# Performance work log

Hardware: AMD Instinct MI355X
Metric: run time of the kernel (lower is better)

Reference implementation:

```python
import jax, jax.numpy as jnp
import numpy as np

N, NFEAT, NHID, NHEADS, NCLASS = 8192, 512, 64, 8, 40
ALPHA = 0.2
NEG = jnp.float32(-9e15)


def _gat_layer(h, W, a, concat):
    # h: [N, Fin], W: [Fin, Fout], a: [2*Fout, 1]
    Fout = W.shape[1]
    Wh = h @ W                      # [N, Fout]
    f1 = Wh @ a[:Fout]              # [N, 1]
    f2 = Wh @ a[Fout:]              # [N, 1]
    e = jax.nn.leaky_relu(f1 + f2.T, negative_slope=ALPHA)  # [N, N]
    # NOTE: source masks on e > 0 (adj is NOT used) - replicate faithfully
    att = jax.nn.softmax(jnp.where(e > 0, e, NEG), axis=1)
    h_prime = att @ Wh              # [N, Fout]
    return jax.nn.elu(h_prime) if concat else h_prime


def setup_inputs() -> dict:
    key = jax.random.key(0)
    ks = jax.random.split(key, 6)
    x = jax.random.normal(ks[0], (N, NFEAT), dtype=jnp.float32)
    adj = jax.random.randint(ks[1], (N, N), 0, 2).astype(jnp.bool_)  # unused by math, kept for fidelity
    s = 0.1
    W_heads = jax.random.normal(ks[2], (NHEADS, NFEAT, NHID), dtype=jnp.float32) * s
    a_heads = jax.random.normal(ks[3], (NHEADS, 2 * NHID, 1), dtype=jnp.float32) * s
    W_out = jax.random.normal(ks[4], (NHID * NHEADS, NCLASS), dtype=jnp.float32) * s
    a_out = jax.random.normal(ks[5], (2 * NCLASS, 1), dtype=jnp.float32) * s
    return {"x": x, "adj": adj, "W_heads": W_heads, "a_heads": a_heads,
            "W_out": W_out, "a_out": a_out}


def reference(x, adj, W_heads, a_heads, W_out, a_out):
    # multi-head GAT layers (concat=True), vmapped over heads
    heads = jax.vmap(lambda W, a: _gat_layer(x, W, a, True))(W_heads, a_heads)  # [H, N, NHID]
    h = jnp.transpose(heads, (1, 0, 2)).reshape(N, NHEADS * NHID)
    # output attention layer (concat=False), then elu + log_softmax
    out = _gat_layer(h, W_out, a_out, False)
    out = jax.nn.elu(out)
    return jax.nn.log_softmax(out, axis=1)
```

## Files before the change

### kernel.cpp

```cpp
#include <hip/hip_runtime.h>
#include <math.h>

#define N_NODES 8192
#define NFEAT 512
#define NHID 64
#define NHEADS 8
#define NCLASS 40
#define NCHUNK 128
#define CHUNK 64
#define NB 4096

using bf16x8 = __attribute__((ext_vector_type(8))) short;
using f32x4 = __attribute__((ext_vector_type(4))) float;

__device__ __forceinline__ ushort f2b(float f) {
  uint u = __builtin_bit_cast(uint, f);
  u += 0x7FFFu + ((u >> 16) & 1u);
  return (ushort)(u >> 16);
}
__device__ __forceinline__ float b2f(ushort h) {
  uint u = (uint)h << 16;
  return __builtin_bit_cast(float, u);
}
__device__ __forceinline__ uint encf(float f) {
  uint u = __builtin_bit_cast(uint, f);
  return u ^ ((u >> 31) ? 0xFFFFFFFFu : 0x80000000u);
}
__device__ __forceinline__ float decf(uint u) {
  u ^= ((u >> 31) ? 0x80000000u : 0xFFFFFFFFu);
  return __builtin_bit_cast(float, u);
}
__device__ __forceinline__ float3 load_rng(const uint* mm, int head) {
  float h = decf(mm[head * 2]);
  float l = decf(~mm[head * 2 + 1]);
  float scale = (float)NB / fmaxf(h - l, 1e-30f);
  return make_float3(l, scale, h);
}
__device__ __forceinline__ int bucket_of(float v, float lo, float scale) {
  float u = fminf(fmaxf((v - lo) * scale, 0.f), (float)(NB - 1));
  return (int)u;
}

__global__ __launch_bounds__(256) void prep_k(const float* __restrict__ W_heads,
                                              ushort* __restrict__ bth,
                                              ushort* __restrict__ btl,
                                              float* __restrict__ zbase,
                                              int zcount) {
  int gid = blockIdx.x * 256 + threadIdx.x;
  int n = gid >> 9, c = gid & 511;
  int h = n >> 6, f = n & 63;
  float w = W_heads[((size_t)h * NFEAT + c) * NHID + f];
  ushort hh = f2b(w);
  bth[gid] = hh;
  btl[gid] = f2b(w - b2f(hh));
  if (gid < zcount) zbase[gid] = 0.f;
}

__global__ __launch_bounds__(256) void gemm1_k(const float* __restrict__ x,
                                               const ushort* __restrict__ bth,
                                               const ushort* __restrict__ btl,
                                               const float* __restrict__ a_heads,
                                               float* __restrict__ Wh,
                                               float* __restrict__ f1,
                                               float* __restrict__ f2,
                                               float* __restrict__ meanS,
                                               uint* __restrict__ mm1) {
  const int row0 = blockIdx.x * 128, col0 = blockIdx.y * 128;
  const int tid = threadIdx.x;
  const int wave = tid >> 6, lane = tid & 63;
  const int wr = wave >> 1, wc = wave & 1;
  __shared__ ushort Ah[128 * 40], Al[128 * 40], Bh[128 * 40], Bl[128 * 40];
  __shared__ float cs[2][64];
  __shared__ uint lmax[2], lmin[2];
  if (tid < 2) { lmax[tid] = 0u; lmin[tid] = 0u; }
  if (tid < 128) cs[tid >> 6][tid & 63] = 0.f;
  f32x4 acc[4][4] = {};
  const int sr = tid >> 1, sh = (tid & 1) * 16;
  const int fr = lane & 15, quad = lane >> 4;
  for (int k0 = 0; k0 < NFEAT; k0 += 32) {
    {
      const float* xs = x + (size_t)(row0 + sr) * NFEAT + k0 + sh;
      float av[16];
      *reinterpret_cast<float4*>(&av[0])  = *reinterpret_cast<const float4*>(xs);
      *reinterpret_cast<float4*>(&av[4])  = *reinterpret_cast<const float4*>(xs + 4);
      *reinterpret_cast<float4*>(&av[8])  = *reinterpret_cast<const float4*>(xs + 8);
      *reinterpret_cast<float4*>(&av[12]) = *reinterpret_cast<const float4*>(xs + 12);
      uint uh[8], ul[8];
#pragma unroll
      for (int q = 0; q < 8; ++q) {
        ushort h0 = f2b(av[2 * q]), h1 = f2b(av[2 * q + 1]);
        ushort l0 = f2b(av[2 * q] - b2f(h0)), l1 = f2b(av[2 * q + 1] - b2f(h1));
        uh[q] = (uint)h0 | ((uint)h1 << 16);
        ul[q] = (uint)l0 | ((uint)l1 << 16);
      }
      *reinterpret_cast<uint4*>(&Ah[sr * 40 + sh])     = make_uint4(uh[0], uh[1], uh[2], uh[3]);
      *reinterpret_cast<uint4*>(&Ah[sr * 40 + sh + 8]) = make_uint4(uh[4], uh[5], uh[6], uh[7]);
      *reinterpret_cast<uint4*>(&Al[sr * 40 + sh])     = make_uint4(ul[0], ul[1], ul[2], ul[3]);
      *reinterpret_cast<uint4*>(&Al[sr * 40 + sh + 8]) = make_uint4(ul[4], ul[5], ul[6], ul[7]);
      size_t boff = (size_t)(col0 + sr) * NFEAT + k0 + sh;
      *reinterpret_cast<uint4*>(&Bh[sr * 40 + sh])     = *reinterpret_cast<const uint4*>(bth + boff);
      *reinterpret_cast<uint4*>(&Bh[sr * 40 + sh + 8]) = *reinterpret_cast<const uint4*>(bth + boff + 8);
      *reinterpret_cast<uint4*>(&Bl[sr * 40 + sh])     = *reinterpret_cast<const uint4*>(btl + boff);
      *reinterpret_cast<uint4*>(&Bl[sr * 40 + sh + 8]) = *reinterpret_cast<const uint4*>(btl + boff + 8);
    }
    __syncthreads();
    bf16x8 afh[4], afl[4], bfh[4], bfl[4];
#pragma unroll
    for (int q = 0; q < 4; ++q) {
      afh[q] = *reinterpret_cast<const bf16x8*>(&Ah[(wr * 64 + q * 16 + fr) * 40 + quad * 8]);
      afl[q] = *reinterpret_cast<const bf16x8*>(&Al[(wr * 64 + q * 16 + fr) * 40 + quad * 8]);
      bfh[q] = *reinterpret_cast<const bf16x8*>(&Bh[(wc * 64 + q * 16 + fr) * 40 + quad * 8]);
      bfl[q] = *reinterpret_cast<const bf16x8*>(&Bl[(wc * 64 + q * 16 + fr) * 40 + quad * 8]);
    }
#pragma unroll
    for (int qr = 0; qr < 4; ++qr)
#pragma unroll
      for (int qc = 0; qc < 4; ++qc) {
        acc[qr][qc] = __builtin_amdgcn_mfma_f32_16x16x32_bf16(afl[qr], bfh[qc], acc[qr][qc], 0, 0, 0);
        acc[qr][qc] = __builtin_amdgcn_mfma_f32_16x16x32_bf16(afh[qr], bfl[qc], acc[qr][qc], 0, 0, 0);
        acc[qr][qc] = __builtin_amdgcn_mfma_f32_16x16x32_bf16(afh[qr], bfh[qc], acc[qr][qc], 0, 0, 0);
      }
    __syncthreads();
  }
  const int head = blockIdx.y * 2 + wc;
#pragma unroll
  for (int qr = 0; qr < 4; ++qr)
#pragma unroll
    for (int qc = 0; qc < 4; ++qc)
#pragma unroll
      for (int i = 0; i < 4; ++i) {
        int row = row0 + wr * 64 + qr * 16 + quad * 4 + i;
        int col = col0 + wc * 64 + qc * 16 + fr;
        Wh[(size_t)row * NFEAT + col] = acc[qr][qc][i];
      }
  const float* ah = a_heads + head * 2 * NHID;
  float a1v[4], a2v[4];
#pragma unroll
  for (int qc = 0; qc < 4; ++qc) { a1v[qc] = ah[qc * 16 + fr]; a2v[qc] = ah[NHID + qc * 16 + fr]; }
#pragma unroll
  for (int qr = 0; qr < 4; ++qr)
#pragma unroll
    for (int i = 0; i < 4; ++i) {
      float s1 = 0.f, s2 = 0.f;
#pragma unroll
      for (int qc = 0; qc < 4; ++qc) { s1 += acc[qr][qc][i] * a1v[qc]; s2 += acc[qr][qc][i] * a2v[qc]; }
#pragma unroll
      for (int m = 1; m < 16; m <<= 1) { s1 += __shfl_xor(s1, m, 64); s2 += __shfl_xor(s2, m, 64); }
      if (fr == 0) {
        int row = row0 + wr * 64 + qr * 16 + quad * 4 + i;
        f1[(head << 13) + row] = s1;
        f2[(head << 13) + row] = s2;
        atomicMax(&lmax[wc], encf(s2));
        atomicMax(&lmin[wc], ~encf(s2));
      }
    }
#pragma unroll
  for (int qc = 0; qc < 4; ++qc) {
    float v = 0.f;
#pragma unroll
    for (int qr = 0; qr < 4; ++qr)
#pragma unroll
      for (int i = 0; i < 4; ++i) v += acc[qr][qc][i];
    v += __shfl_xor(v, 16, 64);
    v += __shfl_xor(v, 32, 64);
    if (quad == 0) atomicAdd(&cs[wc][qc * 16 + fr], v);
  }
  __syncthreads();
  if (tid < 128) atomicAdd(&meanS[(blockIdx.y * 2 + (tid >> 6)) * NHID + (tid & 63)], cs[tid >> 6][tid & 63]);
  if (tid < 2) {
    atomicMax(&mm1[(blockIdx.y * 2 + tid) * 2], lmax[tid]);
    atomicMax(&mm1[(blockIdx.y * 2 + tid) * 2 + 1], lmin[tid]);
  }
}

__global__ __launch_bounds__(256) void gemm2_k(const float* __restrict__ H,
                                               const float* __restrict__ Wout,
                                               const float* __restrict__ a_out,
                                               float* __restrict__ Wh2,
                                               float* __restrict__ f1b,
                                               float* __restrict__ f2b,
                                               float* __restrict__ meanS2,
                                               uint* __restrict__ mm2) {
  const int row0 = blockIdx.x * 32;
  const int tid = threadIdx.x;
  __shared__ float As[32][33];
  __shared__ float Bs[32][40];
  __shared__ float cs[NCLASS];
  __shared__ uint lmax, lmin;
  if (tid < NCLASS) cs[tid] = 0.f;
  if (tid == 0) { lmax = 0u; lmin = 0u; }
  const int m = tid >> 3;
  const int n0 = (tid & 7) * 5;
  float acc[5] = {};
  for (int k0 = 0; k0 < NFEAT; k0 += 32) {
    {
      int kk = tid & 31, mq = tid >> 5;
#pragma unroll
      for (int r = 0; r < 4; ++r)
        As[kk][mq * 4 + r] = H[(size_t)(row0 + mq * 4 + r) * NFEAT + k0 + kk];
    }
    {
#pragma unroll
      for (int r = 0; r < 5; ++r) {
        int idx = tid + r * 256;
        if (idx < 1280) {
          int c = idx / 40, n = idx - c * 40;
          Bs[c][n] = Wout[(size_t)(k0 + c) * NCLASS + n];
        }
      }
    }
    __syncthreads();
#pragma unroll
    for (int kk = 0; kk < 32; ++kk) {
      float a = As[kk][m];
#pragma unroll
      for (int q = 0; q < 5; ++q) acc[q] += a * Bs[kk][n0 + q];
    }
    __syncthreads();
  }
#pragma unroll
  for (int q = 0; q < 5; ++q) Wh2[(size_t)(row0 + m) * NCLASS + n0 + q] = acc[q];
  float p1 = 0.f, p2 = 0.f;
#pragma unroll
  for (int q = 0; q < 5; ++q) {
    p1 += acc[q] * a_out[n0 + q];
    p2 += acc[q] * a_out[NCLASS + n0 + q];
  }
  p1 += __shfl_xor(p1, 1, 64); p1 += __shfl_xor(p1, 2, 64); p1 += __shfl_xor(p1, 4, 64);
  p2 += __shfl_xor(p2, 1, 64); p2 += __shfl_xor(p2, 2, 64); p2 += __shfl_xor(p2, 4, 64);
  if ((tid & 7) == 0) {
    f1b[row0 + m] = p1;
    f2b[row0 + m] = p2;
    atomicMax(&lmax, encf(p2));
    atomicMax(&lmin, ~encf(p2));
  }
#pragma unroll
  for (int q = 0; q < 5; ++q) atomicAdd(&cs[n0 + q], acc[q]);
  __syncthreads();
  if (tid < NCLASS) atomicAdd(&meanS2[tid], cs[tid]);
  if (tid == 0) { atomicMax(&mm2[0], lmax); atomicMax(&mm2[1], lmin); }
}

__global__ __launch_bounds__(256) void hist_k(const float* __restrict__ f2, const uint* __restrict__ mm,
                                              int* __restrict__ hist) {
  int gid = blockIdx.x * 256 + threadIdx.x;
  int head = gid >> 13;
  float3 rg = load_rng(mm, head);
  atomicAdd(&hist[head * NB + bucket_of(f2[gid], rg.x, rg.y)], 1);
}

__global__ __launch_bounds__(1024) void prefix_k(const int* __restrict__ hist, int* __restrict__ bs) {
  __shared__ int sb[NB];
  int head = blockIdx.x, tid = threadIdx.x;
#pragma unroll
  for (int r = 0; r < NB / 1024; ++r) sb[tid + r * 1024] = hist[head * NB + tid + r * 1024];
  __syncthreads();
  for (int st = 1; st < NB; st <<= 1) {
    int v[NB / 1024];
#pragma unroll
    for (int r = 0; r < NB / 1024; ++r) { int i = tid + r * 1024; v[r] = (i >= st) ? sb[i - st] : 0; }
    __syncthreads();
#pragma unroll
    for (int r = 0; r < NB / 1024; ++r) sb[tid + r * 1024] += v[r];
    __syncthreads();
  }
#pragma unroll
  for (int r = 0; r < NB / 1024; ++r) {
    int b = tid + r * 1024;
    bs[head * (NB + 1) + b] = b ? sb[b - 1] : 0;
  }
  if (tid == 0) bs[head * (NB + 1) + NB] = sb[NB - 1];
}

__global__ __launch_bounds__(256) void scat_k(const float* __restrict__ f2, const uint* __restrict__ mm,
                                              const int* __restrict__ bs, int* __restrict__ cnt,
                                              int* __restrict__ idxs, float* __restrict__ f2s,
                                              float* __restrict__ g) {
  int gid = blockIdx.x * 256 + threadIdx.x;
  int head = gid >> 13, i = gid & 8191;
  float v = f2[gid];
  float3 rg = load_rng(mm, head);
  int b = bucket_of(v, rg.x, rg.y);
  int pos = bs[head * (NB + 1) + b] + atomicAdd(&cnt[head * NB + b], 1);
  int base = head << 13;
  idxs[base + pos] = i;
  f2s[base + pos] = v;
  g[base + pos] = expf(v - rg.z);
}

template <int F, int LD, int COLSTEP>
__global__ __launch_bounds__(256) void scanA_k(const float* __restrict__ Wh,
                                               const float* __restrict__ g,
                                               const int* __restrict__ idxs,
                                               float* __restrict__ S,
                                               float* __restrict__ D,
                                               float* __restrict__ T_,
                                               float* __restrict__ Td) {
  constexpr int PAD = (F == 64) ? 66 : 42;
  const int head = blockIdx.y, chunk = blockIdx.x;
  const int tid = threadIdx.x, w = tid >> 6, lane = tid & 63;
  const int base = head << 13;
  const int kbase = base + chunk * CHUNK;
  __shared__ float Sloc[64][PAD];
  __shared__ float Dloc[64];
  __shared__ float wtot[4][PAD];
  __shared__ float wtotD[4];
  int myj = 0; float myg = 0.f;
  if (lane < 16) {
    myj = idxs[kbase + w * 16 + lane];
    myg = g[kbase + w * 16 + lane];
  }
  float acc = 0.f, accD = 0.f;
#pragma unroll
  for (int kk = 15; kk >= 0; --kk) {
    int j = __shfl(myj, kk, 64);
    float gk = __shfl(myg, kk, 64);
    float wv = (lane < F) ? Wh[(size_t)j * LD + head * COLSTEP + lane] : 0.f;
    acc += gk * wv;
    accD += gk;
    if (lane < F) Sloc[w * 16 + kk][lane] = acc;
    if (lane == 0) Dloc[w * 16 + kk] = accD;
  }
  if (lane < F) wtot[w][lane] = acc;
  if (lane == 0) wtotD[w] = accD;
  __syncthreads();
  float off = 0.f, offD = 0.f;
#pragma unroll
  for (int w2 = 1; w2 < 4; ++w2) {
    if (w + w2 < 4) {
      off += (lane < F) ? wtot[w + w2][lane] : 0.f;
      offD += wtotD[w + w2];
    }
  }
#pragma unroll
  for (int kk = 0; kk < 16; ++kk) {
    int e = w * 16 + kk;
    if (lane < F) S[(size_t)(kbase + e) * F + lane] = Sloc[e][lane] + off;
    if (lane == 0) D[kbase + e] = Dloc[e] + offD;
  }
  if (w == 0) {
    if (lane < F) T_[(size_t)(head * NCHUNK + chunk) * F + lane] = wtot[0][lane] + off;
    if (lane == 0) Td[head * NCHUNK + chunk] = wtotD[0] + offD;
  }
}

template <int F>
__global__ __launch_bounds__(1024) void scanB_k(float* __restrict__ T_, float* __restrict__ Td) {
  __shared__ float s[NCHUNK * F];
  __shared__ float td[NCHUNK];
  int head = blockIdx.x;
  int tid = threadIdx.x, slot = tid >> 6, lane = tid & 63;
#pragma unroll
  for (int r = 0; r < 8; ++r) {
    int c = r * 16 + slot;
    if (lane < F) s[c * F + lane] = T_[(size_t)(head * NCHUNK + c) * F + lane];
  }
  if (tid < NCHUNK) td[tid] = Td[head * NCHUNK + tid];
  __syncthreads();
  for (int st = 1; st < NCHUNK; st <<= 1) {
    float v[8];
    float tv = 0.f;
#pragma unroll
    for (int r = 0; r < 8; ++r) {
      int c = r * 16 + slot;
      v[r] = (lane < F && c + st < NCHUNK) ? s[(c + st) * F + lane] : 0.f;
    }
    if (tid < NCHUNK && tid + st < NCHUNK) tv = td[tid + st];
    __syncthreads();
#pragma unroll
    for (int r = 0; r < 8; ++r) {
      int c = r * 16 + slot;
      if (lane < F) s[c * F + lane] += v[r];
    }
    if (tid < NCHUNK) td[tid] += tv;
    __syncthreads();
  }
#pragma unroll
  for (int r = 0; r < 8; ++r) {
    int c = r * 16 + slot;
    if (lane < F) T_[(size_t)(head * NCHUNK + c) * F + lane] = s[c * F + lane];
  }
  if (tid < NCHUNK) Td[head * NCHUNK + tid] = td[tid];
}

__global__ __launch_bounds__(256) void query1_k(const float* __restrict__ f1,
                                                const float* __restrict__ f2s,
                                                const int* __restrict__ idxs,
                                                const float* __restrict__ Wh,
                                                const float* __restrict__ S,
                                                const float* __restrict__ D,
                                                const float* __restrict__ T_,
                                                const float* __restrict__ Td,
                                                const uint* __restrict__ mm,
                                                const int* __restrict__ bs,
                                                const float* __restrict__ meanS,
                                                float* __restrict__ H) {
  int w = blockIdx.x * 4 + (threadIdx.x >> 6);
  int lane = threadIdx.x & 63;
  int head = w & 7, i = w >> 3, base = head << 13;
  float t = f1[base + i];
  float3 rg = load_rng(mm, head);
  int B0 = bucket_of(-t, rg.x, rg.y);
  int p0 = bs[head * (NB + 1) + B0], p1 = bs[head * (NB + 1) + B0 + 1];
  float num = 0.f, den = 0.f;
  int cnt = N_NODES - p1;
  if (p1 < N_NODES) {
    int c = p1 >> 6;
    num = S[(size_t)(base + p1) * NHID + lane] +
          ((c + 1 < NCHUNK) ? T_[(size_t)(head * NCHUNK + c + 1) * NHID + lane] : 0.f);
    den = D[base + p1] + ((c + 1 < NCHUNK) ? Td[head * NCHUNK + c + 1] : 0.f);
  }
  for (int p = p0; p < p1; ++p) {
    float v = f2s[base + p];
    if (t + v > 0.f) {
      int j = idxs[base + p];
      float gk = expf(v - rg.z);
      num += gk * Wh[(size_t)j * NFEAT + head * NHID + lane];
      den += gk;
      ++cnt;
    }
  }
  float val = cnt ? num / den : meanS[head * NHID + lane] * (1.f / N_NODES);
  H[(size_t)i * NFEAT + head * NHID + lane] = (val > 0.f) ? val : expm1f(val);
}

__global__ __launch_bounds__(256) void final_k(const float* __restrict__ f1b,
                                               const float* __restrict__ f2bs,
                                               const int* __restrict__ idx2,
                                               const float* __restrict__ Wh2,
                                               const float* __restrict__ S2,
                                               const float* __restrict__ D2,
                                               const float* __restrict__ T2,
                                               const float* __restrict__ Td2,
                                               const uint* __restrict__ mm2,
                                               const int* __restrict__ bs2,
                                               const float* __restrict__ meanS2,
                                               float* __restrict__ out) {
  int i = blockIdx.x * 4 + (threadIdx.x >> 6);
  int lane = threadIdx.x & 63;
  float t = f1b[i];
  float3 rg = load_rng(mm2, 0);
  int B0 = bucket_of(-t, rg.x, rg.y);
  int p0 = bs2[B0], p1 = bs2[B0 + 1];
  float num = 0.f, den = 0.f;
  int cnt = N_NODES - p1;
  if (p1 < N_NODES) {
    int c = p1 >> 6;
    num = (lane < NCLASS) ? (S2[(size_t)p1 * NCLASS + lane] +
                             ((c + 1 < NCHUNK) ? T2[(size_t)(c + 1) * NCLASS + lane] : 0.f))
                          : 0.f;
    den = D2[p1] + ((c + 1 < NCHUNK) ? Td2[c + 1] : 0.f);
  }
  for (int p = p0; p < p1; ++p) {
    float v = f2bs[p];
    if (t + v > 0.f) {
      int j = idx2[p];
      float gk = expf(v - rg.z);
      if (lane < NCLASS) num += gk * Wh2[(size_t)j * NCLASS + lane];
      den += gk;
      ++cnt;
    }
  }
  float o;
  if (lane < NCLASS) {
    float val = cnt ? num / den : meanS2[lane] * (1.f / N_NODES);
    o = (val > 0.f) ? val : expm1f(val);
  } else {
    o = -INFINITY;
  }
  float m = o;
#pragma unroll
  for (int msk = 32; msk; msk >>= 1) m = fmaxf(m, __shfl_xor(m, msk, 64));
  float e = (lane < NCLASS) ? expf(o - m) : 0.f;
#pragma unroll
  for (int msk = 32; msk; msk >>= 1) e += __shfl_xor(e, msk, 64);
  if (lane < NCLASS) out[(size_t)i * NCLASS + lane] = o - m - logf(e);
}

extern "C" void kernel_launch(void* const* d_in, const int* in_sizes, int n_in,
                              void* d_out, int out_size, void* d_ws, size_t ws_size,
                              hipStream_t stream) {
  const float* x       = (const float*)d_in[0];
  const float* W_heads = (const float*)d_in[2];
  const float* a_heads = (const float*)d_in[3];
  const float* W_out   = (const float*)d_in[4];
  const float* a_out   = (const float*)d_in[5];
  float* out = (float*)d_out;

  float* ws = (float*)d_ws;
  size_t o = 0;
  auto alloc = [&](size_t n) { float* p = ws + o; o += (n + 3) & ~(size_t)3; return p; };
  float*  S1     = alloc((size_t)NHEADS * N_NODES * NHID);
  ushort* BTh    = (ushort*)alloc((size_t)NFEAT * NFEAT / 2);
  ushort* BTl    = (ushort*)alloc((size_t)NFEAT * NFEAT / 2);
  float*  Wh     = alloc((size_t)N_NODES * NFEAT);
  float*  H      = alloc((size_t)N_NODES * NFEAT);
  float*  f1     = alloc(NHEADS * N_NODES);
  float*  f2     = alloc(NHEADS * N_NODES);
  float*  f2s    = alloc(NHEADS * N_NODES);
  int*    idxs   = (int*)alloc(NHEADS * N_NODES);
  float*  g1     = alloc(NHEADS * N_NODES);
  float*  D1     = alloc(NHEADS * N_NODES);
  float*  T1     = alloc(NHEADS * NCHUNK * NHID);
  float*  Td1    = alloc(NHEADS * NCHUNK);
  int*    bst1   = (int*)alloc(NHEADS * (NB + 1));
  float*  Wh2    = alloc((size_t)N_NODES * NCLASS);
  float*  S2     = alloc((size_t)N_NODES * NCLASS);
  float*  f1b    = alloc(N_NODES);
  float*  f2b    = alloc(N_NODES);
  float*  f2bs   = alloc(N_NODES);
  int*    idx2   = (int*)alloc(N_NODES);
  float*  g2     = alloc(N_NODES);
  float*  D2     = alloc(N_NODES);
  float*  T2     = alloc(NCHUNK * NCLASS);
  float*  Td2    = alloc(NCHUNK);
  int*    bst2   = (int*)alloc(NB + 1);
  float*  zbase  = ws + o;
  int*    hist1  = (int*)alloc((size_t)NHEADS * NB);
  int*    cnt1   = (int*)alloc((size_t)NHEADS * NB);
  int*    hist2  = (int*)alloc(NB);
  int*    cnt2   = (int*)alloc(NB);
  uint*   mm1    = (uint*)alloc(16);
  uint*   mm2    = (uint*)alloc(4);
  float*  meanS1 = alloc(NHEADS * NHID);
  float*  meanS2 = alloc(64);
  int zcount = (int)((ws + o) - zbase);

  prep_k<<<1024, 256, 0, stream>>>(W_heads, BTh, BTl, zbase, zcount);
  gemm1_k<<<dim3(64, 4), 256, 0, stream>>>(x, BTh, BTl, a_heads, Wh, f1, f2, meanS1, mm1);
  hist_k<<<(NHEADS * N_NODES) / 256, 256, 0, stream>>>(f2, mm1, hist1);
  prefix_k<<<NHEADS, 1024, 0, stream>>>(hist1, bst1);
  scat_k<<<(NHEADS * N_NODES) / 256, 256, 0, stream>>>(f2, mm1, bst1, cnt1, idxs, f2s, g1);
  scanA_k<NHID, NFEAT, NHID><<<dim3(NCHUNK, NHEADS), 256, 0, stream>>>(Wh, g1, idxs, S1, D1, T1, Td1);
  scanB_k<NHID><<<NHEADS, 1024, 0, stream>>>(T1, Td1);
  query1_k<<<16384, 256, 0, stream>>>(f1, f2s, idxs, Wh, S1, D1, T1, Td1, mm1, bst1, meanS1, H);

  gemm2_k<<<256, 256, 0, stream>>>(H, W_out, a_out, Wh2, f1b, f2b, meanS2, mm2);
  hist_k<<<N_NODES / 256, 256, 0, stream>>>(f2b, mm2, hist2);
  prefix_k<<<1, 1024, 0, stream>>>(hist2, bst2);
  scat_k<<<N_NODES / 256, 256, 0, stream>>>(f2b, mm2, bst2, cnt2, idx2, f2bs, g2);
  scanA_k<NCLASS, NCLASS, 0><<<dim3(NCHUNK, 1), 256, 0, stream>>>(Wh2, g2, idx2, S2, D2, T2, Td2);
  scanB_k<NCLASS><<<1, 1024, 0, stream>>>(T2, Td2);
  final_k<<<2048, 256, 0, stream>>>(f1b, f2bs, idx2, Wh2, S2, D2, T2, Td2, mm2, bst2, meanS2, out);
}
```

Baseline: 535.8 us.

## Fuse histogram/prefix/scatter into one bucket kernel and fold chunk scan via last-block

Replaces the three-kernel bucket sort (global histogram, prefix, scatter) with a single per-head 1024-thread kernel that builds the histogram in shared memory, scans it, and scatters with shared-memory atomics. It also merges the second-level chunk-total scan into the first-level scan kernel, using a threadfence and atomic counter so the last-finishing block does the cross-chunk scan. This removes several launches and global atomic traffic. In exchange, bucketing now runs on only one block per head, which limits parallelism, and the last-block scan is serialized onto a single 256-thread block.

```diff
diff --git a/kernel.cpp b/kernel.cpp
--- a/kernel.cpp
+++ b/kernel.cpp
@@ -241,70 +241,81 @@
   if (tid == 0) { atomicMax(&mm2[0], lmax); atomicMax(&mm2[1], lmin); }
 }
 
-__global__ __launch_bounds__(256) void hist_k(const float* __restrict__ f2, const uint* __restrict__ mm,
-                                              int* __restrict__ hist) {
-  int gid = blockIdx.x * 256 + threadIdx.x;
-  int head = gid >> 13;
+__global__ __launch_bounds__(1024) void bucket_k(const float* __restrict__ f2,
+                                                 const uint* __restrict__ mm,
+                                                 int* __restrict__ bs,
+                                                 int* __restrict__ idxs,
+                                                 float* __restrict__ f2s,
+                                                 float* __restrict__ g) {
+  __shared__ int sb[NB];
+  const int head = blockIdx.x, tid = threadIdx.x;
+  const int base = head * N_NODES;
   float3 rg = load_rng(mm, head);
-  atomicAdd(&hist[head * NB + bucket_of(f2[gid], rg.x, rg.y)], 1);
-}
-
-__global__ __launch_bounds__(1024) void prefix_k(const int* __restrict__ hist, int* __restrict__ bs) {
-  __shared__ int sb[NB];
-  int head = blockIdx.x, tid = threadIdx.x;
-#pragma unroll
-  for (int r = 0; r < NB / 1024; ++r) sb[tid + r * 1024] = hist[head * NB + tid + r * 1024];
+#pragma unroll
+  for (int r = 0; r < NB / 1024; ++r) sb[tid + r * 1024] = 0;
+  __syncthreads();
+  float v[8];
+  int bk[8];
+#pragma unroll
+  for (int r = 0; r < 8; ++r) {
+    v[r] = f2[base + tid + r * 1024];
+    bk[r] = bucket_of(v[r], rg.x, rg.y);
+    atomicAdd(&sb[bk[r]], 1);
+  }
   __syncthreads();
   for (int st = 1; st < NB; st <<= 1) {
-    int v[NB / 1024];
-#pragma unroll
-    for (int r = 0; r < NB / 1024; ++r) { int i = tid + r * 1024; v[r] = (i >= st) ? sb[i - st] : 0; }
-    __syncthreads();
-#pragma unroll
-    for (int r = 0; r < NB / 1024; ++r) sb[tid + r * 1024] += v[r];
-    __syncthreads();
-  }
+    int t[NB / 1024];
+#pragma unroll
+    for (int r = 0; r < NB / 1024; ++r) { int i = tid + r * 1024; t[r] = (i >= st) ? sb[i - st] : 0; }
+    __syncthreads();
+#pragma unroll
+    for (int r = 0; r < NB / 1024; ++r) sb[tid + r * 1024] += t[r];
+    __syncthreads();
+  }
+  int ex[NB / 1024];
 #pragma unroll
   for (int r = 0; r < NB / 1024; ++r) {
     int b = tid + r * 1024;
-    bs[head * (NB + 1) + b] = b ? sb[b - 1] : 0;
+    ex[r] = b ? sb[b - 1] : 0;
+    bs[head * (NB + 1) + b] = ex[r];
   }
   if (tid == 0) bs[head * (NB + 1) + NB] = sb[NB - 1];
-}
-
-__global__ __launch_bounds__(256) void scat_k(const float* __restrict__ f2, const uint* __restrict__ mm,
-                                              const int* __restrict__ bs, int* __restrict__ cnt,
-                                              int* __restrict__ idxs, float* __restrict__ f2s,
-                                              float* __restrict__ g) {
-  int gid = blockIdx.x * 256 + threadIdx.x;
-  int head = gid >> 13, i = gid & 8191;
-  float v = f2[gid];
-  float3 rg = load_rng(mm, head);
-  int b = bucket_of(v, rg.x, rg.y);
-  int pos = bs[head * (NB + 1) + b] + atomicAdd(&cnt[head * NB + b], 1);
-  int base = head << 13;
-  idxs[base + pos] = i;
-  f2s[base + pos] = v;
-  g[base + pos] = expf(v - rg.z);
+  __syncthreads();
+#pragma unroll
+  for (int r = 0; r < NB / 1024; ++r) sb[tid + r * 1024] = ex[r];
+  __syncthreads();
+#pragma unroll
+  for (int r = 0; r < 8; ++r) {
+    int pos = atomicAdd(&sb[bk[r]], 1);
+    int i = tid + r * 1024;
+    idxs[base + pos] = i;
+    f2s[base + pos] = v[r];
+    g[base + pos] = expf(v[r] - rg.z);
+  }
 }
 
 template <int F, int LD, int COLSTEP>
-__global__ __launch_bounds__(256) void scanA_k(const float* __restrict__ Wh,
-                                               const float* __restrict__ g,
-                                               const int* __restrict__ idxs,
-                                               float* __restrict__ S,
-                                               float* __restrict__ D,
-                                               float* __restrict__ T_,
-                                               float* __restrict__ Td) {
+__global__ __launch_bounds__(256) void scanAB_k(const float* __restrict__ Wh,
+                                                const float* __restrict__ g,
+                                                const int* __restrict__ idxs,
+                                                float* __restrict__ S,
+                                                float* __restrict__ D,
+                                                float* __restrict__ T_,
+                                                float* __restrict__ Td,
+                                                int* __restrict__ cntA) {
   constexpr int PAD = (F == 64) ? 66 : 42;
+  constexpr int SZ1 = 64 * PAD + 4 * PAD + 64 + 4;
+  constexpr int SZ2 = NCHUNK * F + NCHUNK;
+  __shared__ float smem[SZ1 > SZ2 ? SZ1 : SZ2];
+  __shared__ int isLast;
+  float (*Sloc)[PAD] = (float(*)[PAD])smem;
+  float* wtot  = smem + 64 * PAD;
+  float* Dloc  = wtot + 4 * PAD;
+  float* wtotD = Dloc + 64;
   const int head = blockIdx.y, chunk = blockIdx.x;
   const int tid = threadIdx.x, w = tid >> 6, lane = tid & 63;
   const int base = head << 13;
   const int kbase = base + chunk * CHUNK;
-  __shared__ float Sloc[64][PAD];
-  __shared__ float Dloc[64];
-  __shared__ float wtot[4][PAD];
-  __shared__ float wtotD[4];
   int myj = 0; float myg = 0.f;
   if (lane < 16) {
     myj = idxs[kbase + w * 16 + lane];
@@ -321,14 +332,14 @@
     if (lane < F) Sloc[w * 16 + kk][lane] = acc;
     if (lane == 0) Dloc[w * 16 + kk] = accD;
   }
-  if (lane < F) wtot[w][lane] = acc;
+  if (lane < F) wtot[w * PAD + lane] = acc;
   if (lane == 0) wtotD[w] = accD;
   __syncthreads();
   float off = 0.f, offD = 0.f;
 #pragma unroll
   for (int w2 = 1; w2 < 4; ++w2) {
     if (w + w2 < 4) {
-      off += (lane < F) ? wtot[w + w2][lane] : 0.f;
+      off += (lane < F) ? wtot[(w + w2) * PAD + lane] : 0.f;
       offD += wtotD[w + w2];
     }
   }
@@ -339,48 +350,37 @@
     if (lane == 0) D[kbase + e] = Dloc[e] + offD;
   }
   if (w == 0) {
-    if (lane < F) T_[(size_t)(head * NCHUNK + chunk) * F + lane] = wtot[0][lane] + off;
+    if (lane < F) T_[(size_t)(head * NCHUNK + chunk) * F + lane] = wtot[lane] + off;
     if (lane == 0) Td[head * NCHUNK + chunk] = wtotD[0] + offD;
   }
-}
-
-template <int F>
-__global__ __launch_bounds__(1024) void scanB_k(float* __restrict__ T_, float* __restrict__ Td) {
-  __shared__ float s[NCHUNK * F];
-  __shared__ float td[NCHUNK];
-  int head = blockIdx.x;
-  int tid = threadIdx.x, slot = tid >> 6, lane = tid & 63;
-#pragma unroll
-  for (int r = 0; r < 8; ++r) {
-    int c = r * 16 + slot;
-    if (lane < F) s[c * F + lane] = T_[(size_t)(head * NCHUNK + c) * F + lane];
-  }
-  if (tid < NCHUNK) td[tid] = Td[head * NCHUNK + tid];
-  __syncthreads();
+  __threadfence();
+  if (tid == 0) isLast = (atomicAdd(&cntA[head], 1) == NCHUNK - 1);
+  __syncthreads();
+  if (!isLast) return;
+  float* s  = smem;
+  float* td = smem + NCHUNK * F;
+  for (int idx = tid; idx < NCHUNK * F; idx += 256) s[idx] = T_[(size_t)head * NCHUNK * F + idx];
+  for (int c = tid; c < NCHUNK; c += 256) td[c] = Td[head * NCHUNK + c];
+  __syncthreads();
+  constexpr int PT = (NCHUNK * F + 255) / 256;
   for (int st = 1; st < NCHUNK; st <<= 1) {
-    float v[8];
-    float tv = 0.f;
-#pragma unroll
-    for (int r = 0; r < 8; ++r) {
-      int c = r * 16 + slot;
-      v[r] = (lane < F && c + st < NCHUNK) ? s[(c + st) * F + lane] : 0.f;
-    }
-    if (tid < NCHUNK && tid + st < NCHUNK) tv = td[tid + st];
-    __syncthreads();
-#pragma unroll
-    for (int r = 0; r < 8; ++r) {
-      int c = r * 16 + slot;
-      if (lane < F) s[c * F + lane] += v[r];
-    }
-    if (tid < NCHUNK) td[tid] += tv;
-    __syncthreads();
-  }
-#pragma unroll
-  for (int r = 0; r < 8; ++r) {
-    int c = r * 16 + slot;
-    if (lane < F) T_[(size_t)(head * NCHUNK + c) * F + lane] = s[c * F + lane];
-  }
-  if (tid < NCHUNK) Td[head * NCHUNK + tid] = td[tid];
+    float tv[PT];
+    int n = 0;
+#pragma unroll
+    for (int idx = tid; idx < NCHUNK * F; idx += 256, ++n) {
+      int c = idx / F;
+      tv[n] = (c + st < NCHUNK) ? s[idx + st * F] : 0.f;
+    }
+    float tdv = (tid < NCHUNK && tid + st < NCHUNK) ? td[tid + st] : 0.f;
+    __syncthreads();
+    n = 0;
+#pragma unroll
+    for (int idx = tid; idx < NCHUNK * F; idx += 256, ++n) s[idx] += tv[n];
+    if (tid < NCHUNK) td[tid] += tdv;
+    __syncthreads();
+  }
+  for (int idx = tid; idx < NCHUNK * F; idx += 256) T_[(size_t)head * NCHUNK * F + idx] = s[idx];
+  for (int c = tid; c < NCHUNK; c += 256) Td[head * NCHUNK + c] = td[c];
 }
 
 __global__ __launch_bounds__(256) void query1_k(const float* __restrict__ f1,
@@ -516,30 +516,22 @@
   float*  Td2    = alloc(NCHUNK);
   int*    bst2   = (int*)alloc(NB + 1);
   float*  zbase  = ws + o;
-  int*    hist1  = (int*)alloc((size_t)NHEADS * NB);
-  int*    cnt1   = (int*)alloc((size_t)NHEADS * NB);
-  int*    hist2  = (int*)alloc(NB);
-  int*    cnt2   = (int*)alloc(NB);
   uint*   mm1    = (uint*)alloc(16);
   uint*   mm2    = (uint*)alloc(4);
   float*  meanS1 = alloc(NHEADS * NHID);
   float*  meanS2 = alloc(64);
+  int*    cntA1  = (int*)alloc(NHEADS);
+  int*    cntA2  = (int*)alloc(4);
   int zcount = (int)((ws + o) - zbase);
 
   prep_k<<<1024, 256, 0, stream>>>(W_heads, BTh, BTl, zbase, zcount);
   gemm1_k<<<dim3(64, 4), 256, 0, stream>>>(x, BTh, BTl, a_heads, Wh, f1, f2, meanS1, mm1);
-  hist_k<<<(NHEADS * N_NODES) / 256, 256, 0, stream>>>(f2, mm1, hist1);
-  prefix_k<<<NHEADS, 1024, 0, stream>>>(hist1, bst1);
-  scat_k<<<(NHEADS * N_NODES) / 256, 256, 0, stream>>>(f2, mm1, bst1, cnt1, idxs, f2s, g1);
-  scanA_k<NHID, NFEAT, NHID><<<dim3(NCHUNK, NHEADS), 256, 0, stream>>>(Wh, g1, idxs, S1, D1, T1, Td1);
-  scanB_k<NHID><<<NHEADS, 1024, 0, stream>>>(T1, Td1);
+  bucket_k<<<NHEADS, 1024, 0, stream>>>(f2, mm1, bst1, idxs, f2s, g1);
+  scanAB_k<NHID, NFEAT, NHID><<<dim3(NCHUNK, NHEADS), 256, 0, stream>>>(Wh, g1, idxs, S1, D1, T1, Td1, cntA1);
   query1_k<<<16384, 256, 0, stream>>>(f1, f2s, idxs, Wh, S1, D1, T1, Td1, mm1, bst1, meanS1, H);
 
   gemm2_k<<<256, 256, 0, stream>>>(H, W_out, a_out, Wh2, f1b, f2b, meanS2, mm2);
-  hist_k<<<N_NODES / 256, 256, 0, stream>>>(f2b, mm2, hist2);
-  prefix_k<<<1, 1024, 0, stream>>>(hist2, bst2);
-  scat_k<<<N_NODES / 256, 256, 0, stream>>>(f2b, mm2, bst2, cnt2, idx2, f2bs, g2);
-  scanA_k<NCLASS, NCLASS, 0><<<dim3(NCHUNK, 1), 256, 0, stream>>>(Wh2, g2, idx2, S2, D2, T2, Td2);
-  scanB_k<NCLASS><<<1, 1024, 0, stream>>>(T2, Td2);
+  bucket_k<<<1, 1024, 0, stream>>>(f2b, mm2, bst2, idx2, f2bs, g2);
+  scanAB_k<NCLASS, NCLASS, 0><<<dim3(NCHUNK, 1), 256, 0, stream>>>(Wh2, g2, idx2, S2, D2, T2, Td2, cntA2);
   final_k<<<2048, 256, 0, stream>>>(f1b, f2bs, idx2, Wh2, S2, D2, T2, Td2, mm2, bst2, meanS2, out);
 }
```

After: 691.0 us. 29.0% more time.

## Fuse histogram, prefix scan and scatter into one per-head bucket kernel

Applied to the files above, without the earlier changes.

Replaces the three bucket-sort kernels (global histogram, prefix scan, atomic scatter) with a single kernel per head. It builds the histogram with shared-memory atomics, scans it in place, and scatters indices using shared-memory counters. This removes four launches and the global hist/cnt buffers along with their zeroing, but the work now runs on only 8 blocks (or 1 block for layer 2), so parallelism is lower.

```diff
diff --git a/kernel.cpp b/kernel.cpp
--- a/kernel.cpp
+++ b/kernel.cpp
@@ -241,51 +241,57 @@
   if (tid == 0) { atomicMax(&mm2[0], lmax); atomicMax(&mm2[1], lmin); }
 }
 
-__global__ __launch_bounds__(256) void hist_k(const float* __restrict__ f2, const uint* __restrict__ mm,
-                                              int* __restrict__ hist) {
-  int gid = blockIdx.x * 256 + threadIdx.x;
-  int head = gid >> 13;
+__global__ __launch_bounds__(1024) void bucket_k(const float* __restrict__ f2,
+                                                 const uint* __restrict__ mm,
+                                                 int* __restrict__ bs,
+                                                 int* __restrict__ idxs,
+                                                 float* __restrict__ f2s,
+                                                 float* __restrict__ g) {
+  __shared__ int sb[NB];
+  const int head = blockIdx.x, tid = threadIdx.x;
+  const int base = head * N_NODES;
   float3 rg = load_rng(mm, head);
-  atomicAdd(&hist[head * NB + bucket_of(f2[gid], rg.x, rg.y)], 1);
-}
-
-__global__ __launch_bounds__(1024) void prefix_k(const int* __restrict__ hist, int* __restrict__ bs) {
-  __shared__ int sb[NB];
-  int head = blockIdx.x, tid = threadIdx.x;
-#pragma unroll
-  for (int r = 0; r < NB / 1024; ++r) sb[tid + r * 1024] = hist[head * NB + tid + r * 1024];
+#pragma unroll
+  for (int r = 0; r < NB / 1024; ++r) sb[tid + r * 1024] = 0;
+  __syncthreads();
+  float v[8];
+  int bk[8];
+#pragma unroll
+  for (int r = 0; r < 8; ++r) {
+    v[r] = f2[base + tid + r * 1024];
+    bk[r] = bucket_of(v[r], rg.x, rg.y);
+    atomicAdd(&sb[bk[r]], 1);
+  }
   __syncthreads();
   for (int st = 1; st < NB; st <<= 1) {
-    int v[NB / 1024];
-#pragma unroll
-    for (int r = 0; r < NB / 1024; ++r) { int i = tid + r * 1024; v[r] = (i >= st) ? sb[i - st] : 0; }
-    __syncthreads();
-#pragma unroll
-    for (int r = 0; r < NB / 1024; ++r) sb[tid + r * 1024] += v[r];
-    __syncthreads();
-  }
+    int t[NB / 1024];
+#pragma unroll
+    for (int r = 0; r < NB / 1024; ++r) { int i = tid + r * 1024; t[r] = (i >= st) ? sb[i - st] : 0; }
+    __syncthreads();
+#pragma unroll
+    for (int r = 0; r < NB / 1024; ++r) sb[tid + r * 1024] += t[r];
+    __syncthreads();
+  }
+  int ex[NB / 1024];
 #pragma unroll
   for (int r = 0; r < NB / 1024; ++r) {
     int b = tid + r * 1024;
-    bs[head * (NB + 1) + b] = b ? sb[b - 1] : 0;
+    ex[r] = b ? sb[b - 1] : 0;
+    bs[head * (NB + 1) + b] = ex[r];
   }
   if (tid == 0) bs[head * (NB + 1) + NB] = sb[NB - 1];
-}
-
-__global__ __launch_bounds__(256) void scat_k(const float* __restrict__ f2, const uint* __restrict__ mm,
-                                              const int* __restrict__ bs, int* __restrict__ cnt,
-                                              int* __restrict__ idxs, float* __restrict__ f2s,
-                                              float* __restrict__ g) {
-  int gid = blockIdx.x * 256 + threadIdx.x;
-  int head = gid >> 13, i = gid & 8191;
-  float v = f2[gid];
-  float3 rg = load_rng(mm, head);
-  int b = bucket_of(v, rg.x, rg.y);
-  int pos = bs[head * (NB + 1) + b] + atomicAdd(&cnt[head * NB + b], 1);
-  int base = head << 13;
-  idxs[base + pos] = i;
-  f2s[base + pos] = v;
-  g[base + pos] = expf(v - rg.z);
+  __syncthreads();
+#pragma unroll
+  for (int r = 0; r < NB / 1024; ++r) sb[tid + r * 1024] = ex[r];
+  __syncthreads();
+#pragma unroll
+  for (int r = 0; r < 8; ++r) {
+    int pos = atomicAdd(&sb[bk[r]], 1);
+    int i = tid + r * 1024;
+    idxs[base + pos] = i;
+    f2s[base + pos] = v[r];
+    g[base + pos] = expf(v[r] - rg.z);
+  }
 }
 
 template <int F, int LD, int COLSTEP>
@@ -516,10 +522,6 @@
   float*  Td2    = alloc(NCHUNK);
   int*    bst2   = (int*)alloc(NB + 1);
   float*  zbase  = ws + o;
-  int*    hist1  = (int*)alloc((size_t)NHEADS * NB);
-  int*    cnt1   = (int*)alloc((size_t)NHEADS * NB);
-  int*    hist2  = (int*)alloc(NB);
-  int*    cnt2   = (int*)alloc(NB);
   uint*   mm1    = (uint*)alloc(16);
   uint*   mm2    = (uint*)alloc(4);
   float*  meanS1 = alloc(NHEADS * NHID);
@@ -528,17 +530,13 @@
 
   prep_k<<<1024, 256, 0, stream>>>(W_heads, BTh, BTl, zbase, zcount);
   gemm1_k<<<dim3(64, 4), 256, 0, stream>>>(x, BTh, BTl, a_heads, Wh, f1, f2, meanS1, mm1);
-  hist_k<<<(NHEADS * N_NODES) / 256, 256, 0, stream>>>(f2, mm1, hist1);
-  prefix_k<<<NHEADS, 1024, 0, stream>>>(hist1, bst1);
-  scat_k<<<(NHEADS * N_NODES) / 256, 256, 0, stream>>>(f2, mm1, bst1, cnt1, idxs, f2s, g1);
+  bucket_k<<<NHEADS, 1024, 0, stream>>>(f2, mm1, bst1, idxs, f2s, g1);
   scanA_k<NHID, NFEAT, NHID><<<dim3(NCHUNK, NHEADS), 256, 0, stream>>>(Wh, g1, idxs, S1, D1, T1, Td1);
   scanB_k<NHID><<<NHEADS, 1024, 0, stream>>>(T1, Td1);
   query1_k<<<16384, 256, 0, stream>>>(f1, f2s, idxs, Wh, S1, D1, T1, Td1, mm1, bst1, meanS1, H);
 
   gemm2_k<<<256, 256, 0, stream>>>(H, W_out, a_out, Wh2, f1b, f2b, meanS2, mm2);
-  hist_k<<<N_NODES / 256, 256, 0, stream>>>(f2b, mm2, hist2);
-  prefix_k<<<1, 1024, 0, stream>>>(hist2, bst2);
-  scat_k<<<N_NODES / 256, 256, 0, stream>>>(f2b, mm2, bst2, cnt2, idx2, f2bs, g2);
+  bucket_k<<<1, 1024, 0, stream>>>(f2b, mm2, bst2, idx2, f2bs, g2);
   scanA_k<NCLASS, NCLASS, 0><<<dim3(NCHUNK, 1), 256, 0, stream>>>(Wh2, g2, idx2, S2, D2, T2, Td2);
   scanB_k<NCLASS><<<1, 1024, 0, stream>>>(T2, Td2);
   final_k<<<2048, 256, 0, stream>>>(f1b, f2bs, idx2, Wh2, S2, D2, T2, Td2, mm2, bst2, meanS2, out);
```

Measured after the change: 536.7 us. Within noise of the previous version (+0.2%).
